# Optimization experiments

Measured on AMD Instinct MI355X. Metric: run time of the kernel, lower is better.

The kernel has to match this reference:

```python
import jax, jax.numpy as jnp
import numpy as np

T, D, K = 16384, 512, 128
NODES = [512, 512]


def _rnn_layer(X, Wx, Wh, bh, h0):
    # X: [T, M1] -> [T, M2]; precompute input projection (parallel part)
    Xp = X @ Wx  # [T, M2]
    def step(h, x):
        h = jax.nn.relu(x + h @ Wh + bh)
        return h, h
    _, out = jax.lax.scan(step, h0[0], Xp)
    return out  # [T, M2]


def setup_inputs() -> dict:
    key = jax.random.key(0)
    ks = jax.random.split(key, 16)
    inp = {"X": jax.random.normal(ks[0], (T, D), dtype=jnp.float32)}
    M1 = D
    for i, M2 in enumerate(NODES):
        s = 1.0 / np.sqrt(M1 + M2)
        inp[f"Wx{i}"] = jax.random.normal(ks[1 + 3 * i], (M1, M2), dtype=jnp.float32) * s
        inp[f"Wh{i}"] = jax.random.normal(ks[2 + 3 * i], (M2, M2), dtype=jnp.float32) * s
        inp[f"bh{i}"] = jnp.zeros((M2,), dtype=jnp.float32)
        inp[f"h0{i}"] = jnp.zeros((1, M2), dtype=jnp.float32)
        M1 = M2
    # nn.Linear(M1, K): weight [K, M1], bias [K]
    lim = 1.0 / np.sqrt(M1)
    inp["W_log"] = jax.random.uniform(ks[10], (K, M1), minval=-lim, maxval=lim, dtype=jnp.float32)
    inp["b_log"] = jax.random.uniform(ks[11], (K,), minval=-lim, maxval=lim, dtype=jnp.float32)
    return inp


def reference(X, Wx0, Wh0, bh0, h00, Wx1, Wh1, bh1, h01, W_log, b_log):
    h = _rnn_layer(X, Wx0, Wh0, bh0, h00)
    h = _rnn_layer(h, Wx1, Wh1, bh1, h01)
    return h @ W_log.T + b_log  # [T, K]
```

## Files before the change

### kernel.cpp

```cpp
#include <hip/hip_runtime.h>
#include <stdint.h>

#define TT 16384
#define DH 512
#define KK 128
#define SENT 0xAAAAAAAAu
#define CROWS 32
#define NCHUNK (TT / CROWS)
#define NPROJ 56
#define RSLOT 16

#define BARRIER_LDS() do { \
    asm volatile("s_waitcnt lgkmcnt(0)" ::: "memory"); \
    __builtin_amdgcn_s_barrier(); \
} while (0)

__device__ uint32_t g_ring[2][RSLOT][DH];
__device__ uint32_t g_flagXp[2][NCHUNK];

static __device__ __forceinline__ uint32_t aload(const uint32_t* p) {
    return __hip_atomic_load(p, __ATOMIC_RELAXED, __HIP_MEMORY_SCOPE_AGENT);
}
static __device__ __forceinline__ void astore(uint32_t* p, uint32_t v) {
    __hip_atomic_store(p, v, __ATOMIC_RELAXED, __HIP_MEMORY_SCOPE_AGENT);
}
static __device__ __forceinline__ float aloadf(const float* p) {
    return __uint_as_float(aload((const uint32_t*)p));
}

__global__ void init_kernel() {
    const int tid = threadIdx.x;
    uint32_t* r = &g_ring[0][0][0];
    for (int i = tid; i < 2 * RSLOT * DH; i += 1024) r[i] = SENT;
    uint32_t* f = &g_flagXp[0][0];
    for (int i = tid; i < 2 * NCHUNK; i += 1024) f[i] = SENT;
}

static __device__ void proj_chunk(const float* __restrict__ W,
                                  const float* __restrict__ src, int srcMode,
                                  float* __restrict__ dst, uint32_t* flag, int t0,
                                  float* inT , float* wt )
{
    const int tid = threadIdx.x;
    #pragma unroll
    for (int i = 0; i < 16; ++i) {
        int idx = tid + 1024 * i;
        int row = idx >> 9;
        int col = idx & 511;
        float v;
        if (srcMode == 0) {
            v = src[(size_t)t0 * DH + idx];
        } else {
            const uint32_t* p = (const uint32_t*)src + (size_t)t0 * DH + idx;
            uint32_t u;
            while ((u = aload(p)) == SENT) __builtin_amdgcn_s_sleep(1);
            v = __uint_as_float(u);
        }
        inT[col * 36 + row] = v;
    }
    __syncthreads();

    const int rg = (tid >> 7) & 7;
    const int cg = tid & 127;
    float acc[4][4] = {{0.f}};

    for (int kt = 0; kt < 16; ++kt) {
        const int k0 = kt * 32;
        #pragma unroll
        for (int i = 0; i < 4; ++i) {
            int f4 = tid + 1024 * i;
            int wr = f4 >> 7;
            int wc = (f4 & 127) << 2;
            *(float4*)&wt[wr * 516 + wc] =
                *(const float4*)&W[(size_t)(k0 + wr) * DH + wc];
        }
        __syncthreads();
        #pragma unroll 8
        for (int kk = 0; kk < 32; ++kk) {
            float4 a = *(const float4*)&inT[(k0 + kk) * 36 + (rg << 2)];
            float4 w = *(const float4*)&wt[kk * 516 + (cg << 2)];
            acc[0][0] += a.x * w.x; acc[0][1] += a.x * w.y; acc[0][2] += a.x * w.z; acc[0][3] += a.x * w.w;
            acc[1][0] += a.y * w.x; acc[1][1] += a.y * w.y; acc[1][2] += a.y * w.z; acc[1][3] += a.y * w.w;
            acc[2][0] += a.z * w.x; acc[2][1] += a.z * w.y; acc[2][2] += a.z * w.z; acc[2][3] += a.z * w.w;
            acc[3][0] += a.w * w.x; acc[3][1] += a.w * w.y; acc[3][2] += a.w * w.z; acc[3][3] += a.w * w.w;
        }
        __syncthreads();
    }
    #pragma unroll
    for (int i = 0; i < 4; ++i)
        #pragma unroll
        for (int j = 0; j < 4; ++j)
            astore((uint32_t*)&dst[(size_t)(t0 + (rg << 2) + i) * DH + (cg << 2) + j],
                   __float_as_uint(acc[i][j]));
    __threadfence();
    __syncthreads();
    if (tid == 0)
        __hip_atomic_store(flag, 1u, __ATOMIC_RELEASE, __HIP_MEMORY_SCOPE_AGENT);
}

__global__ __launch_bounds__(1024, 1)
void fused(const float* __restrict__ X,
           const float* __restrict__ Wx0, const float* __restrict__ Wh0,
           const float* __restrict__ bh0, const float* __restrict__ h00,
           const float* __restrict__ Wx1, const float* __restrict__ Wh1,
           const float* __restrict__ bh1, const float* __restrict__ h01,
           float* H0r, float* H1r)
{
    __shared__ __align__(16) float s_hbuf[DH];
    __shared__ float s_part[8][128];
    __shared__ __align__(16) float s_inT[DH * 36];
    __shared__ __align__(16) float s_wt[32 * 516];

    const int bIdx = blockIdx.x;
    const int m8 = bIdx & 7;
    const int tid = threadIdx.x;

    if (bIdx < 32 && m8 < 2) {
        const int L = m8;
        const int b = bIdx >> 3;
        const int c = tid >> 7;
        const int o = tid & 127;
        const int og = (b << 7) + o;

        const float* Wh  = L ? Wh1 : Wh0;
        const float* bhv = L ? bh1 : bh0;
        const float* h0v = L ? h01 : h00;
        float* Hful      = L ? H1r : H0r;
        const float* Xp  = L ? H0r : H1r;
        uint32_t* ring         = &g_ring[L][0][0];
        uint32_t* flagXp       = &g_flagXp[L][0];

        float wh[64];
        #pragma unroll
        for (int j = 0; j < 64; ++j)
            wh[j] = Wh[(size_t)((c << 6) + j) * DH + og];
        const float bias = bhv[og];

        const int ptid = (tid + 1024 - ((b << 8) + 256)) & 1023;
        const bool isPoll = ptid < 384;
        const int pcol = (ptid < (b << 7)) ? ptid : ptid + 128;
        const bool isSelf = (c >> 1) == b;
        const bool isRed = tid < 128;

        if (tid < DH) s_hbuf[tid] = h0v[tid];

        float xp_next = 0.f;
        int curCh = -1;
        if (isRed) {
            while (__hip_atomic_load(&flagXp[0], __ATOMIC_ACQUIRE,
                                     __HIP_MEMORY_SCOPE_AGENT) != 1u)
                __builtin_amdgcn_s_sleep(1);
            curCh = 0;
            xp_next = aloadf(&Xp[og]);
        }
        __syncthreads();

        for (int t = 0; t < TT; ++t) {
            if (t > 0 && isPoll) {
                const uint32_t par = (uint32_t)((t - 1) >> 4) & 1u;
                const uint32_t* p = &ring[(((t - 1) & 15) << 9) + pcol];
                uint32_t v;
                do { v = aload(p); } while ((v >> 31) != par);
                s_hbuf[pcol] = __uint_as_float(v & 0x7fffffffu);
            }
            float acc = 0.f;
            if (isSelf | (t == 0)) {
                const float4* h4 = (const float4*)&s_hbuf[c << 6];
                #pragma unroll
                for (int j4 = 0; j4 < 16; ++j4) {
                    float4 hv = h4[j4];
                    acc += wh[4*j4+0]*hv.x + wh[4*j4+1]*hv.y
                         + wh[4*j4+2]*hv.z + wh[4*j4+3]*hv.w;
                }
                s_part[c][o] = acc;
            }
            BARRIER_LDS();
            if (!(isSelf | (t == 0))) {
                const float4* h4 = (const float4*)&s_hbuf[c << 6];
                #pragma unroll
                for (int j4 = 0; j4 < 16; ++j4) {
                    float4 hv = h4[j4];
                    acc += wh[4*j4+0]*hv.x + wh[4*j4+1]*hv.y
                         + wh[4*j4+2]*hv.z + wh[4*j4+3]*hv.w;
                }
                s_part[c][o] = acc;
            }
            BARRIER_LDS();
            if (isRed) {
                float v = bias + xp_next;
                #pragma unroll
                for (int cc = 0; cc < 8; ++cc) v += s_part[cc][o];
                v = fmaxf(v, 0.f);
                const uint32_t hb = __float_as_uint(v);
                astore(&ring[((t & 15) << 9) + og],
                       hb | (((uint32_t)(t >> 4) & 1u) << 31));
                astore((uint32_t*)Hful + (size_t)t * DH + og, hb);
                s_hbuf[og] = v;
                if (t + 1 < TT) {
                    const int ch = (t + 1) >> 5;
                    if (ch != curCh) {
                        while (__hip_atomic_load(&flagXp[ch], __ATOMIC_ACQUIRE,
                                                 __HIP_MEMORY_SCOPE_AGENT) != 1u) {}
                        curCh = ch;
                    }
                    xp_next = aloadf(&Xp[(size_t)(t + 1) * DH + og]);
                }
            }
            BARRIER_LDS();
        }
    } else {
        const int pi = (bIdx < 32) ? (((bIdx >> 3) * 6) + (m8 - 2))
                                   : (24 + (bIdx - 32));
        for (int cc = pi; cc < NCHUNK; cc += NPROJ) {
            proj_chunk(Wx0, X,   0, H1r , &g_flagXp[0][cc], cc * CROWS, s_inT, s_wt);
            proj_chunk(Wx1, H0r, 1, H0r , &g_flagXp[1][cc], cc * CROWS, s_inT, s_wt);
        }
    }
}

__global__ __launch_bounds__(128, 1)
void logits_kernel(const float* __restrict__ H1, const float* __restrict__ Wl,
                   const float* __restrict__ bl, float* __restrict__ out)
{
    const int t0 = blockIdx.x * 8;
    const int k = threadIdx.x;

    __shared__ __align__(16) float hs[8 * DH];
    for (int idx = k; idx < 8 * DH / 4; idx += 128)
        ((float4*)hs)[idx] = ((const float4*)&H1[(size_t)t0 * DH])[idx];
    __syncthreads();

    float acc[8];
    const float bk = bl[k];
    #pragma unroll
    for (int r = 0; r < 8; ++r) acc[r] = bk;

    const float4* w4 = (const float4*)&Wl[(size_t)k * DH];
    for (int j = 0; j < DH / 4; ++j) {
        float4 w = w4[j];
        #pragma unroll
        for (int r = 0; r < 8; ++r) {
            float4 h = ((const float4*)&hs[r * DH])[j];
            acc[r] += w.x * h.x + w.y * h.y + w.z * h.z + w.w * h.w;
        }
    }
    #pragma unroll
    for (int r = 0; r < 8; ++r) out[(size_t)(t0 + r) * KK + k] = acc[r];
}

extern "C" void kernel_launch(void* const* d_in, const int* in_sizes, int n_in,
                              void* d_out, int out_size, void* d_ws, size_t ws_size,
                              hipStream_t stream)
{
    const float* X   = (const float*)d_in[0];
    const float* Wx0 = (const float*)d_in[1];
    const float* Wh0 = (const float*)d_in[2];
    const float* bh0 = (const float*)d_in[3];
    const float* h00 = (const float*)d_in[4];
    const float* Wx1 = (const float*)d_in[5];
    const float* Wh1 = (const float*)d_in[6];
    const float* bh1 = (const float*)d_in[7];
    const float* h01 = (const float*)d_in[8];
    const float* Wl  = (const float*)d_in[9];
    const float* bl  = (const float*)d_in[10];
    float* out = (float*)d_out;

    float* H0r = (float*)d_ws;
    float* H1r = H0r + (size_t)TT * DH;

    hipMemsetAsync(d_ws, 0xAA, (size_t)TT * DH * sizeof(float), stream);
    hipLaunchKernelGGL(init_kernel, dim3(1), dim3(1024), 0, stream);
    hipLaunchKernelGGL(fused, dim3(64), dim3(1024), 0, stream,
                       X, Wx0, Wh0, bh0, h00, Wx1, Wh1, bh1, h01, H0r, H1r);
    hipLaunchKernelGGL(logits_kernel, dim3(TT / 8), dim3(128), 0, stream,
                       H1r, Wl, bl, out);
}
```

Baseline: 20.19 ms.

## Co-locate recurrent blocks on one XCD and exchange hidden state through L2

Each block reads its XCD id from a hardware register and registers itself in a global table. A grid-wide rendezvous then assigns the 8 recurrent roles to blocks that share one XCD, and all remaining blocks become projection workers. The per-step hidden-state ring is now written twice: once with sc0 stores meant to stay in the shared L2 for fast same-XCD polling, and once through device-scope atomics as a fallback. This targets the cross-die coherence latency of the per-timestep handoff, at the cost of a startup spin barrier that needs all 64 blocks co-resident, extra stores per step, and reliance on undocumented cache-scope behaviour.

```diff
diff --git a/kernel.cpp b/kernel.cpp
--- a/kernel.cpp
+++ b/kernel.cpp
@@ -15,8 +15,12 @@
     __builtin_amdgcn_s_barrier(); \
 } while (0)
 
-__device__ uint32_t g_ring[2][RSLOT][DH];
+__device__ uint32_t g_ringF[2][RSLOT][DH];
+__device__ uint32_t g_ringM[2][RSLOT][DH];
 __device__ uint32_t g_flagXp[2][NCHUNK];
+__device__ uint32_t g_cnt[8];
+__device__ uint32_t g_total;
+__device__ uint32_t g_members[8][64];
 
 static __device__ __forceinline__ uint32_t aload(const uint32_t* p) {
     return __hip_atomic_load(p, __ATOMIC_RELAXED, __HIP_MEMORY_SCOPE_AGENT);
@@ -28,12 +32,28 @@
     return __uint_as_float(aload((const uint32_t*)p));
 }
 
+static __device__ __forceinline__ uint32_t l2load(const uint32_t* p) {
+    uint32_t v;
+    asm volatile("global_load_dword %0, %1, off sc0\n\ts_waitcnt vmcnt(0)"
+                 : "=&v"(v) : "v"(p) : "memory");
+    return v;
+}
+static __device__ __forceinline__ void l2store(uint32_t* p, uint32_t v) {
+    asm volatile("global_store_dword %0, %1, off sc0" :: "v"(p), "v"(v) : "memory");
+}
+
 __global__ void init_kernel() {
     const int tid = threadIdx.x;
-    uint32_t* r = &g_ring[0][0][0];
-    for (int i = tid; i < 2 * RSLOT * DH; i += 1024) r[i] = SENT;
+    uint32_t* rf = &g_ringF[0][0][0];
+    for (int i = tid; i < 2 * RSLOT * DH; i += 1024) rf[i] = SENT;
+    uint32_t* rm = &g_ringM[0][0][0];
+    for (int i = tid; i < 2 * RSLOT * DH; i += 1024) rm[i] = SENT;
     uint32_t* f = &g_flagXp[0][0];
     for (int i = tid; i < 2 * NCHUNK; i += 1024) f[i] = SENT;
+    uint32_t* m = &g_members[0][0];
+    for (int i = tid; i < 8 * 64; i += 1024) m[i] = 0xFFFFFFFFu;
+    if (tid < 8) g_cnt[tid] = 0u;
+    if (tid == 0) g_total = 0u;
 }
 
 static __device__ void proj_chunk(const float* __restrict__ W,
@@ -110,14 +130,50 @@
     __shared__ float s_part[8][128];
     __shared__ __align__(16) float s_inT[DH * 36];
     __shared__ __align__(16) float s_wt[32 * 516];
+    __shared__ int s_role;
+    __shared__ int s_fast;
 
     const int bIdx = blockIdx.x;
-    const int m8 = bIdx & 7;
     const int tid = threadIdx.x;
 
-    if (bIdx < 32 && m8 < 2) {
-        const int L = m8;
-        const int b = bIdx >> 3;
+    if (tid == 0) {
+        uint32_t xcd = ((uint32_t)__builtin_amdgcn_s_getreg((31 << 11) | 20)) & 7u;
+        uint32_t slot = __hip_atomic_fetch_add(&g_cnt[xcd], 1u, __ATOMIC_RELAXED,
+                                               __HIP_MEMORY_SCOPE_AGENT);
+        astore(&g_members[xcd][slot & 63u], (uint32_t)bIdx);
+        __hip_atomic_fetch_add(&g_total, 1u, __ATOMIC_RELEASE,
+                               __HIP_MEMORY_SCOPE_AGENT);
+        while (__hip_atomic_load(&g_total, __ATOMIC_ACQUIRE,
+                                 __HIP_MEMORY_SCOPE_AGENT) < 64u)
+            __builtin_amdgcn_s_sleep(2);
+        uint32_t cnt[8];
+        for (int x = 0; x < 8; ++x) cnt[x] = aload(&g_cnt[x]);
+        int star = 0;
+        for (int x = 0; x < 8; ++x) { if (cnt[x] >= 8u) { star = x; break; } }
+        int role = -1;
+        for (int s = 0; s < 8; ++s)
+            if (aload(&g_members[star][s]) == (uint32_t)bIdx) role = s;
+        if (role < 0) {
+            int pi = 0;
+            for (int x = 0; x < 8; ++x) {
+                const uint32_t cx = cnt[x] > 64u ? 64u : cnt[x];
+                for (uint32_t s = 0; s < cx; ++s) {
+                    if (x == star && s < 8u) continue;
+                    if (role < 0 &&
+                        aload(&g_members[x][s]) == (uint32_t)bIdx) role = 8 + pi;
+                    ++pi;
+                }
+            }
+        }
+        s_role = role;
+        s_fast = 1;
+    }
+    __syncthreads();
+    const int role = s_role;
+
+    if (role >= 0 && role < 8) {
+        const int L = role >> 2;
+        const int b = role & 3;
         const int c = tid >> 7;
         const int o = tid & 127;
         const int og = (b << 7) + o;
@@ -127,7 +183,8 @@
         const float* h0v = L ? h01 : h00;
         float* Hful      = L ? H1r : H0r;
         const float* Xp  = L ? H0r : H1r;
-        uint32_t* ring         = &g_ring[L][0][0];
+        uint32_t* ringF        = &g_ringF[L][0][0];
+        uint32_t* ringM        = &g_ringM[L][0][0];
         uint32_t* flagXp       = &g_flagXp[L][0];
 
         float wh[64];
@@ -158,9 +215,19 @@
         for (int t = 0; t < TT; ++t) {
             if (t > 0 && isPoll) {
                 const uint32_t par = (uint32_t)((t - 1) >> 4) & 1u;
-                const uint32_t* p = &ring[(((t - 1) & 15) << 9) + pcol];
+                const int idx = (((t - 1) & 15) << 9) + pcol;
                 uint32_t v;
-                do { v = aload(p); } while ((v >> 31) != par);
+                bool got = false;
+                if (s_fast) {
+                    for (int it = 0; it < 64; ++it) {
+                        v = l2load(&ringF[idx]);
+                        if ((v >> 31) == par) { got = true; break; }
+                    }
+                    if (!got) s_fast = 0;
+                }
+                if (!got) {
+                    do { v = aload(&ringM[idx]); } while ((v >> 31) != par);
+                }
                 s_hbuf[pcol] = __uint_as_float(v & 0x7fffffffu);
             }
             float acc = 0.f;
@@ -192,8 +259,10 @@
                 for (int cc = 0; cc < 8; ++cc) v += s_part[cc][o];
                 v = fmaxf(v, 0.f);
                 const uint32_t hb = __float_as_uint(v);
-                astore(&ring[((t & 15) << 9) + og],
-                       hb | (((uint32_t)(t >> 4) & 1u) << 31));
+                const uint32_t tag = hb | (((uint32_t)(t >> 4) & 1u) << 31);
+                const int ridx = ((t & 15) << 9) + og;
+                l2store(&ringF[ridx], tag);
+                astore(&ringM[ridx], tag);
                 astore((uint32_t*)Hful + (size_t)t * DH + og, hb);
                 s_hbuf[og] = v;
                 if (t + 1 < TT) {
@@ -209,8 +278,7 @@
             BARRIER_LDS();
         }
     } else {
-        const int pi = (bIdx < 32) ? (((bIdx >> 3) * 6) + (m8 - 2))
-                                   : (24 + (bIdx - 32));
+        const int pi = role - 8;
         for (int cc = pi; cc < NCHUNK; cc += NPROJ) {
             proj_chunk(Wx0, X,   0, H1r , &g_flagXp[0][cc], cc * CROWS, s_inT, s_wt);
             proj_chunk(Wx1, H0r, 1, H0r , &g_flagXp[1][cc], cc * CROWS, s_inT, s_wt);
```

Result: no change. 19.99 ms (-1.0%).
